# Performance work log

Hardware: AMD Instinct MI355X
Metric: run time of the kernel (lower is better)

## Reference

```python
import jax, jax.numpy as jnp
import numpy as np

HID = 256
NUM_ENT = 100000
NUM_REL = 50
E = 320000  # edges per direction; edge_index has 2*E columns
BN_EPS = 1e-5


def setup_inputs() -> dict:
    key = jax.random.key(0)
    ks = jax.random.split(key, 10)
    x = jax.random.normal(ks[0], (NUM_ENT, HID), dtype=jnp.float32)
    edge_index = jax.random.randint(ks[1], (2, 2 * E), 0, NUM_ENT)
    edge_type = jax.random.randint(ks[2], (2 * E,), 0, NUM_REL)
    rel_embed = jax.random.normal(ks[3], (NUM_REL, HID), dtype=jnp.float32)
    # xavier_normal init: std = sqrt(2 / (fan_in + fan_out))
    w_std = (2.0 / (HID + HID)) ** 0.5
    w_loop = jax.random.normal(ks[4], (HID, HID), dtype=jnp.float32) * w_std
    w_in = jax.random.normal(ks[5], (HID, HID), dtype=jnp.float32) * w_std
    w_out = jax.random.normal(ks[6], (HID, HID), dtype=jnp.float32) * w_std
    w_rel = jax.random.normal(ks[7], (HID, HID), dtype=jnp.float32) * w_std
    loop_rel = jax.random.normal(ks[8], (1, HID), dtype=jnp.float32) * ((2.0 / (1 + HID)) ** 0.5)
    bn_weight = jnp.ones((HID,), dtype=jnp.float32)
    bn_bias = jnp.zeros((HID,), dtype=jnp.float32)
    return {
        "x": x, "edge_index": edge_index, "edge_type": edge_type,
        "rel_embed": rel_embed, "w_loop": w_loop, "w_in": w_in,
        "w_out": w_out, "w_rel": w_rel, "loop_rel": loop_rel,
        "bn_weight": bn_weight, "bn_bias": bn_bias,
    }


def _compute_norm(edge_index, num_ent):
    # symmetric D^-1/2 * D^-1/2 norm; degree counted on row (target) index
    row, col = edge_index[0], edge_index[1]
    deg = jax.ops.segment_sum(jnp.ones_like(row, dtype=jnp.float32), row, num_segments=num_ent)
    deg_inv = jnp.where(deg > 0, deg ** -0.5, 0.0)
    return deg_inv[row] * deg_inv[col]


def _propagate(x, idx, etype, rel_all, W, norm, num_ent):
    # gather source nodes (idx[1]), compose with relation emb (mult), transform, scale, scatter-add to targets (idx[0])
    msg = (x[idx[1]] * rel_all[etype]) @ W  # [E, d]
    if norm is not None:
        msg = msg * norm[:, None]
    return jax.ops.segment_sum(msg, idx[0], num_segments=num_ent)


def reference(x, edge_index, edge_type, rel_embed, w_loop, w_in, w_out, w_rel,
              loop_rel, bn_weight, bn_bias):
    num_ent = x.shape[0]
    rel_all = jnp.concatenate([rel_embed, loop_rel], axis=0)  # [R+1, d]
    e = edge_index.shape[1] // 2
    in_index, out_index = edge_index[:, :e], edge_index[:, e:]
    in_type, out_type = edge_type[:e], edge_type[e:]

    in_norm = _compute_norm(in_index, num_ent)
    out_norm = _compute_norm(out_index, num_ent)

    in_res = _propagate(x, in_index, in_type, rel_all, w_in, in_norm, num_ent)
    out_res = _propagate(x, out_index, out_type, rel_all, w_out, out_norm, num_ent)
    # self-loop: identity scatter -> just per-node compose+transform
    loop_res = (x * loop_rel) @ w_loop

    out = (in_res + out_res + loop_res) * (1.0 / 3.0)

    # BatchNorm1d in training mode (batch stats, biased variance)
    mean = out.mean(axis=0)
    var = out.var(axis=0)
    out = (out - mean) * jax.lax.rsqrt(var + BN_EPS) * bn_weight + bn_bias

    rel_out = (rel_all @ w_rel)[:-1]  # drop loop relation
    return out, rel_out
```

## Files before the change

kernel.cpp:

```cpp
#include <hip/hip_runtime.h>

#define HID     256
#define N_ENT   100000
#define TOT_E   640000
#define HALF_E  320000
#define NSEG    (2 * N_ENT)
#define BN_EPSF 1e-5f
#define SCAN_ELEMS 1024
#define NBLK_SCAN  ((NSEG + SCAN_ELEMS - 1) / SCAN_ELEMS)

typedef short bf16x8 __attribute__((ext_vector_type(8)));
typedef short bf16x4 __attribute__((ext_vector_type(4)));
typedef float f32x4  __attribute__((ext_vector_type(4)));

__device__ __forceinline__ short f2b(float f) {
    union { float f; unsigned u; } c; c.f = f;
    unsigned u = c.u;
    u += 0x7FFF + ((u >> 16) & 1);
    return (short)(u >> 16);
}
__device__ __forceinline__ float b2f(short b) {
    union { unsigned u; float f; } c;
    c.u = ((unsigned)(unsigned short)b) << 16;
    return c.f;
}
__device__ __forceinline__ void gload16(const void* g, void* l) {
    __builtin_amdgcn_global_load_lds(
        (const __attribute__((address_space(1))) unsigned*)(g),
        (__attribute__((address_space(3))) unsigned*)(l), 16, 0, 0);
}

__global__ void hist_kernel(const int* __restrict__ ei, int* __restrict__ offs) {
    int j = blockIdx.x * 256 + threadIdx.x;
    if (j >= TOT_E) return;
    int seg = ei[j] + ((j < HALF_E) ? 0 : N_ENT);
    atomicAdd(&offs[seg], 1);
}

__global__ __launch_bounds__(256) void scan1(int* __restrict__ offs, int* __restrict__ bsums,
                                             float* __restrict__ rnorm) {
    __shared__ int tsum[256];
    int b = blockIdx.x, t = threadIdx.x;
    int base = b * SCAN_ELEMS + t * 4;
    int v[4] = {0, 0, 0, 0};
    if (base + 3 < NSEG) {
        int4 lv = *(const int4*)(offs + base);
        v[0] = lv.x; v[1] = lv.y; v[2] = lv.z; v[3] = lv.w;
    } else {
        for (int i = 0; i < 4; ++i) if (base + i < NSEG) v[i] = offs[base + i];
    }
    #pragma unroll
    for (int i = 0; i < 4; ++i)
        if (base + i < NSEG)
            rnorm[base + i] = (v[i] > 0) ? rsqrtf((float)v[i]) : 0.f;
    tsum[t] = v[0] + v[1] + v[2] + v[3];
    __syncthreads();
    for (int d = 1; d < 256; d <<= 1) {
        int val = (t >= d) ? tsum[t - d] : 0;
        __syncthreads();
        tsum[t] += val;
        __syncthreads();
    }
    int run = (t == 0) ? 0 : tsum[t - 1];
    if (t == 255) bsums[b] = tsum[255];
    int w[4];
    for (int i = 0; i < 4; ++i) { w[i] = run; run += v[i]; }
    if (base + 3 < NSEG) *(int4*)(offs + base) = make_int4(w[0], w[1], w[2], w[3]);
    else for (int i = 0; i < 4; ++i) if (base + i < NSEG) offs[base + i] = w[i];
}

__global__ void scan2(int* __restrict__ bsums) {
    __shared__ int tmp[256];
    int t = threadIdx.x;
    int v = (t < NBLK_SCAN) ? bsums[t] : 0;
    tmp[t] = v;
    __syncthreads();
    for (int d = 1; d < 256; d <<= 1) {
        int val = (t >= d) ? tmp[t - d] : 0;
        __syncthreads();
        tmp[t] += val;
        __syncthreads();
    }
    if (t < NBLK_SCAN) bsums[t] = (t == 0) ? 0 : tmp[t - 1];
}

__global__ __launch_bounds__(256) void scan3(int* __restrict__ offs, const int* __restrict__ bsums) {
    int b = blockIdx.x;
    int add = bsums[b];
    int base = b * SCAN_ELEMS + threadIdx.x * 4;
    if (base + 3 < NSEG) {
        int4 v = *(int4*)(offs + base);
        v.x += add; v.y += add; v.z += add; v.w += add;
        *(int4*)(offs + base) = v;
    } else {
        for (int i = 0; i < 4; ++i) if (base + i < NSEG) offs[base + i] += add;
    }
}

__global__ void fill8_kernel(const int* __restrict__ ei, const int* __restrict__ et,
                             int* __restrict__ offs, const float* __restrict__ rnorm,
                             int2* __restrict__ elist8) {
    int j = blockIdx.x * 256 + threadIdx.x;
    if (j >= TOT_E) return;
    int hb  = (j < HALF_E) ? 0 : N_ENT;
    int seg = ei[j] + hb;
    int col = ei[TOT_E + j];
    float norm = rnorm[seg] * rnorm[hb + col];
    int pos = atomicAdd(&offs[seg], 1);
    elist8[pos] = make_int2(col | (et[j] << 17), __float_as_int(norm));
}

__global__ void tobf16_kernel(const float* __restrict__ src, short* __restrict__ dst, int n8) {
    int i = blockIdx.x * 256 + threadIdx.x;
    if (i >= n8) return;
    const float4* p = (const float4*)(src + (size_t)i * 8);
    float4 v0 = p[0], v1 = p[1];
    bf16x8 pk;
    pk[0]=f2b(v0.x); pk[1]=f2b(v0.y); pk[2]=f2b(v0.z); pk[3]=f2b(v0.w);
    pk[4]=f2b(v1.x); pk[5]=f2b(v1.y); pk[6]=f2b(v1.z); pk[7]=f2b(v1.w);
    *(bf16x8*)(dst + (size_t)i * 8) = pk;
}

__global__ __launch_bounds__(256) void gather_h(
        const short* __restrict__ xh, const short* __restrict__ relh,
        const int* __restrict__ offs, const int2* __restrict__ elist8,
        short* __restrict__ accA, short* __restrict__ accB) {
    int s = blockIdx.x * 8 + (threadIdx.x >> 5);
    int lane = threadIdx.x & 31;
    int start = (s == 0) ? 0 : offs[s - 1];
    int end   = offs[s];
    float a0[8], a1[8];
    #pragma unroll
    for (int k = 0; k < 8; ++k) { a0[k] = 0.f; a1[k] = 0.f; }
    int e = start;
    for (; e + 2 <= end; e += 2) {
        int2 p0 = elist8[e];
        int2 p1 = elist8[e + 1];
        int   c0 = p0.x & 0x1FFFF, t0 = p0.x >> 17;
        float n0 = __int_as_float(p0.y);
        int   c1 = p1.x & 0x1FFFF, t1 = p1.x >> 17;
        float n1 = __int_as_float(p1.y);
        bf16x8 xv0 = *(const bf16x8*)(xh   + (size_t)c0 * HID + lane * 8);
        bf16x8 rv0 = *(const bf16x8*)(relh + (size_t)t0 * HID + lane * 8);
        bf16x8 xv1 = *(const bf16x8*)(xh   + (size_t)c1 * HID + lane * 8);
        bf16x8 rv1 = *(const bf16x8*)(relh + (size_t)t1 * HID + lane * 8);
        #pragma unroll
        for (int k = 0; k < 8; ++k) {
            a0[k] += b2f(xv0[k]) * b2f(rv0[k]) * n0;
            a1[k] += b2f(xv1[k]) * b2f(rv1[k]) * n1;
        }
    }
    if (e < end) {
        int2 p = elist8[e];
        int   c = p.x & 0x1FFFF, t = p.x >> 17;
        float n = __int_as_float(p.y);
        bf16x8 xv = *(const bf16x8*)(xh   + (size_t)c * HID + lane * 8);
        bf16x8 rv = *(const bf16x8*)(relh + (size_t)t * HID + lane * 8);
        #pragma unroll
        for (int k = 0; k < 8; ++k)
            a0[k] += b2f(xv[k]) * b2f(rv[k]) * n;
    }
    int hb = (s >= N_ENT) ? N_ENT : 0;
    short* dst = ((s >= N_ENT) ? accB : accA) + (size_t)(s - hb) * HID + lane * 8;
    bf16x8 pk;
    #pragma unroll
    for (int k = 0; k < 8; ++k) pk[k] = f2b(a0[k] + a1[k]);
    *(bf16x8*)dst = pk;
}

__global__ void wcat_kernel(const float* __restrict__ w_in, const float* __restrict__ w_out,
                            const float* __restrict__ w_loop, const float* __restrict__ loop_rel,
                            short* __restrict__ WT) {
    int n = blockIdx.x;
    int t = threadIdx.x;
    float v0 = w_in  [(size_t)t * HID + n];
    float v1 = w_out [(size_t)t * HID + n];
    float v2 = w_loop[(size_t)t * HID + n] * loop_rel[t];
    short* row = WT + (size_t)n * 768;
    row[t]       = f2b(v0);
    row[256 + t] = f2b(v1);
    row[512 + t] = f2b(v2);
}

template <bool BF16OUT>
__global__ __launch_bounds__(256) void gemm_mfma_db(
        const short* __restrict__ accA, const short* __restrict__ accB,
        const short* __restrict__ xh, const short* __restrict__ WT,
        float* __restrict__ out, short* __restrict__ outh, float* __restrict__ stats)
{
    __shared__ __align__(16) short As[2][64 * 64];
    __shared__ __align__(16) short Bs[2][256 * 64];
    const int tid = threadIdx.x;
    const int l   = tid & 63;
    const int wid = tid >> 6;
    const int r0  = blockIdx.x * 64;
    const int lr  = l & 15;
    const int lg  = l >> 4;

    f32x4 acc[4][4];
    #pragma unroll
    for (int i = 0; i < 4; ++i)
        #pragma unroll
        for (int j = 0; j < 4; ++j)
            acc[i][j] = (f32x4){0.f, 0.f, 0.f, 0.f};

    auto stage = [&](int buf, int kt) {
        const int src = kt >> 2;
        const short* Ap = (src == 0) ? accA : ((src == 1) ? accB : xh);
        const int ksl = (kt & 3) * 64;
        const int ksg = kt * 64;
        #pragma unroll
        for (int h = 0; h < 2; ++h) {
            int c  = wid * 2 + h;
            int r  = c * 8 + (l >> 3);
            int sg = (l & 7) ^ (r & 7);
            int gr = r0 + r;
            if (gr >= N_ENT) gr = N_ENT - 1;
            gload16(Ap + (size_t)gr * HID + ksl + sg * 8, &As[buf][c * 512]);
        }
        #pragma unroll
        for (int i = 0; i < 8; ++i) {
            int c  = wid * 8 + i;
            int n  = c * 8 + (l >> 3);
            int sg = (l & 7) ^ (n & 7);
            gload16(WT + (size_t)n * 768 + ksg + sg * 8, &Bs[buf][c * 512]);
        }
    };

    stage(0, 0);
    __syncthreads();
    int cur = 0;
    for (int kt = 0; kt < 12; ++kt) {
        if (kt < 11) stage(cur ^ 1, kt + 1);
        #pragma unroll
        for (int kc = 0; kc < 2; ++kc) {
            const int gsel = kc * 4 + lg;
            bf16x8 af[4], bfr[4];
            #pragma unroll
            for (int i = 0; i < 4; ++i) {
                int r = 16 * i + lr;
                af[i] = *(const bf16x8*)&As[cur][r * 64 + (gsel ^ (r & 7)) * 8];
            }
            #pragma unroll
            for (int j = 0; j < 4; ++j) {
                int n = wid * 64 + 16 * j + lr;
                bfr[j] = *(const bf16x8*)&Bs[cur][n * 64 + (gsel ^ (n & 7)) * 8];
            }
            #pragma unroll
            for (int i = 0; i < 4; ++i)
                #pragma unroll
                for (int j = 0; j < 4; ++j)
                    acc[i][j] = __builtin_amdgcn_mfma_f32_16x16x32_bf16(
                                    af[i], bfr[j], acc[i][j], 0, 0, 0);
        }
        __syncthreads();
        cur ^= 1;
    }

    const float third = 1.f / 3.f;
    float s[4]  = {0.f, 0.f, 0.f, 0.f};
    float sq[4] = {0.f, 0.f, 0.f, 0.f};
    #pragma unroll
    for (int i = 0; i < 4; ++i) {
        #pragma unroll
        for (int v = 0; v < 4; ++v) {
            int grow = r0 + 16 * i + lg * 4 + v;
            if (grow < N_ENT) {
                #pragma unroll
                for (int j = 0; j < 4; ++j) {
                    float val = acc[i][j][v] * third;
                    int col = wid * 64 + 16 * j + lr;
                    if (BF16OUT) outh[(size_t)grow * HID + col] = f2b(val);
                    else         out [(size_t)grow * HID + col] = val;
                    s[j] += val; sq[j] += val * val;
                }
            }
        }
    }
    #pragma unroll
    for (int j = 0; j < 4; ++j) {
        s[j]  += __shfl_xor(s[j], 16);  s[j]  += __shfl_xor(s[j], 32);
        sq[j] += __shfl_xor(sq[j], 16); sq[j] += __shfl_xor(sq[j], 32);
    }
    if (lg == 0) {
        #pragma unroll
        for (int j = 0; j < 4; ++j) {
            int c = wid * 64 + 16 * j + lr;
            atomicAdd(&stats[c], s[j]);
            atomicAdd(&stats[HID + c], sq[j]);
        }
    }
}

__global__ void bn_apply_h(const short* __restrict__ outh, float* __restrict__ out,
                           const float* __restrict__ stats,
                           const float* __restrict__ bnw, const float* __restrict__ bnb) {
    const float invN = 1.f / (float)N_ENT;
    const int total8 = N_ENT * (HID / 8);
    for (int i = blockIdx.x * 256 + threadIdx.x; i < total8; i += gridDim.x * 256) {
        int c = (i & 31) * 8;
        bf16x8 v = *(const bf16x8*)(outh + (size_t)i * 8);
        float r[8];
        #pragma unroll
        for (int k = 0; k < 8; ++k) {
            float mean = stats[c + k] * invN;
            float var  = stats[HID + c + k] * invN - mean * mean;
            float sc   = rsqrtf(var + BN_EPSF) * bnw[c + k];
            float sh   = bnb[c + k] - mean * sc;
            r[k] = b2f(v[k]) * sc + sh;
        }
        float4* dst = (float4*)(out + (size_t)i * 8);
        dst[0] = make_float4(r[0], r[1], r[2], r[3]);
        dst[1] = make_float4(r[4], r[5], r[6], r[7]);
    }
}

__global__ void bn_apply(float* __restrict__ out, const float* __restrict__ stats,
                         const float* __restrict__ bnw, const float* __restrict__ bnb) {
    const float invN = 1.f / (float)N_ENT;
    const int total4 = N_ENT * (HID / 4);
    for (int i = blockIdx.x * 256 + threadIdx.x; i < total4; i += gridDim.x * 256) {
        int c = (i & 63) * 4;
        float4 v = *(float4*)(out + (size_t)i * 4);
        #pragma unroll
        for (int k = 0; k < 4; ++k) {
            float mean = stats[c + k] * invN;
            float var  = stats[HID + c + k] * invN - mean * mean;
            float sc   = rsqrtf(var + BN_EPSF) * bnw[c + k];
            float sh   = bnb[c + k] - mean * sc;
            float* comp = (k == 0) ? &v.x : (k == 1) ? &v.y : (k == 2) ? &v.z : &v.w;
            *comp = (*comp) * sc + sh;
        }
        *(float4*)(out + (size_t)i * 4) = v;
    }
}

__global__ void relout_kernel(const float* __restrict__ rel_embed,
                              const float* __restrict__ w_rel,
                              float* __restrict__ rel_out) {
    __shared__ float row[HID];
    int r = blockIdx.x;
    int c = threadIdx.x;
    row[c] = rel_embed[(size_t)r * HID + c];
    __syncthreads();
    float s = 0.f;
    for (int k = 0; k < HID; ++k) s += row[k] * w_rel[(size_t)k * HID + c];
    rel_out[(size_t)r * HID + c] = s;
}

extern "C" void kernel_launch(void* const* d_in, const int* in_sizes, int n_in,
                              void* d_out, int out_size, void* d_ws, size_t ws_size,
                              hipStream_t stream) {
    const float* x        = (const float*)d_in[0];
    const int*   ei       = (const int*)d_in[1];
    const int*   et       = (const int*)d_in[2];
    const float* rel      = (const float*)d_in[3];
    const float* w_loop   = (const float*)d_in[4];
    const float* w_in     = (const float*)d_in[5];
    const float* w_out    = (const float*)d_in[6];
    const float* w_rel    = (const float*)d_in[7];
    const float* loop_rel = (const float*)d_in[8];
    const float* bnw      = (const float*)d_in[9];
    const float* bnb      = (const float*)d_in[10];

    float* out     = (float*)d_out;
    float* rel_out = out + (size_t)N_ENT * HID;

    const size_t XH_B   = (size_t)N_ENT * HID * 2;
    const size_t ACC_B  = (size_t)N_ENT * HID * 2;
    const size_t OFFS_B = (size_t)NSEG * 4;
    const size_t EL8_B  = (size_t)TOT_E * 8;
    const size_t RN_B   = (size_t)NSEG * 4;
    const size_t RELH_B = (size_t)50 * HID * 2;
    const size_t base_need = XH_B + 2 * ACC_B + OFFS_B + EL8_B + RN_B
                           + 256 * 4 + 512 * 4 + RELH_B;
    const size_t OUTH_B = (size_t)N_ENT * HID * 2;
    const bool   have_outh = (ws_size >= base_need + OUTH_B);

    char* w = (char*)d_ws;
    short* xh     = (short*)w;              w += XH_B;
    short* accA_h = (short*)w;              w += ACC_B;
    short* accB_h = (short*)w;              w += ACC_B;
    int*   offs   = (int*)w;                w += OFFS_B;
    int2*  elist8 = (int2*)w;               short* WT = (short*)w;   w += EL8_B;
    float* rnorm  = (float*)w;              w += RN_B;
    int*   bsums  = (int*)w;                w += 256 * 4;
    float* stats  = (float*)w;              w += 512 * 4;
    short* relh   = (short*)w;              w += RELH_B;
    short* outh   = (short*)w;

    hipMemsetAsync(offs, 0, OFFS_B, stream);
    hipMemsetAsync(stats, 0, 512 * 4, stream);

    tobf16_kernel<<<(N_ENT * HID / 8 + 255) / 256, 256, 0, stream>>>(x, xh, N_ENT * HID / 8);
    tobf16_kernel<<<(50 * HID / 8 + 255) / 256, 256, 0, stream>>>(rel, relh, 50 * HID / 8);
    hist_kernel<<<TOT_E / 256, 256, 0, stream>>>(ei, offs);
    scan1<<<NBLK_SCAN, 256, 0, stream>>>(offs, bsums, rnorm);
    scan2<<<1, 256, 0, stream>>>(bsums);
    scan3<<<NBLK_SCAN, 256, 0, stream>>>(offs, bsums);
    fill8_kernel<<<TOT_E / 256, 256, 0, stream>>>(ei, et, offs, rnorm, elist8);
    gather_h<<<NSEG / 8, 256, 0, stream>>>(xh, relh, offs, elist8, accA_h, accB_h);
    wcat_kernel<<<256, 256, 0, stream>>>(w_in, w_out, w_loop, loop_rel, WT);
    if (have_outh) {
        gemm_mfma_db<true><<<(N_ENT + 63) / 64, 256, 0, stream>>>(
            accA_h, accB_h, xh, WT, out, outh, stats);
        bn_apply_h<<<2048, 256, 0, stream>>>(outh, out, stats, bnw, bnb);
    } else {
        gemm_mfma_db<false><<<(N_ENT + 63) / 64, 256, 0, stream>>>(
            accA_h, accB_h, xh, WT, out, outh, stats);
        bn_apply<<<2048, 256, 0, stream>>>(out, stats, bnw, bnb);
    }
    relout_kernel<<<50, 256, 0, stream>>>(rel, w_rel, rel_out);
}
```

Measured before the change: 319.3 us.

## Shrink GEMM K-tile, unroll gather by four, merge scan and conversion kernels

Several changes land together. The GEMM K-step drops from 64 to 32, which halves shared memory per block to allow higher occupancy, at the cost of twice as many barriered iterations. The gather loop now handles four edges per iteration to raise memory-level parallelism. The conversion kernels and the scan2/scan3 pair are each fused into one kernel to cut launches, with every scan3 block redoing the small block-sum scan. The BN apply grid is halved and the relout inner loop is unrolled.

```diff
diff --git a/kernel.cpp b/kernel.cpp
--- a/kernel.cpp
+++ b/kernel.cpp
@@ -10,7 +10,6 @@
 #define NBLK_SCAN  ((NSEG + SCAN_ELEMS - 1) / SCAN_ELEMS)
 
 typedef short bf16x8 __attribute__((ext_vector_type(8)));
-typedef short bf16x4 __attribute__((ext_vector_type(4)));
 typedef float f32x4  __attribute__((ext_vector_type(4)));
 
 __device__ __forceinline__ short f2b(float f) {
@@ -69,11 +68,10 @@
     else for (int i = 0; i < 4; ++i) if (base + i < NSEG) offs[base + i] = w[i];
 }
 
-__global__ void scan2(int* __restrict__ bsums) {
+__global__ __launch_bounds__(256) void scan3f(int* __restrict__ offs, const int* __restrict__ bsums) {
     __shared__ int tmp[256];
-    int t = threadIdx.x;
-    int v = (t < NBLK_SCAN) ? bsums[t] : 0;
-    tmp[t] = v;
+    int b = blockIdx.x, t = threadIdx.x;
+    tmp[t] = (t < NBLK_SCAN) ? bsums[t] : 0;
     __syncthreads();
     for (int d = 1; d < 256; d <<= 1) {
         int val = (t >= d) ? tmp[t - d] : 0;
@@ -81,13 +79,8 @@
         tmp[t] += val;
         __syncthreads();
     }
-    if (t < NBLK_SCAN) bsums[t] = (t == 0) ? 0 : tmp[t - 1];
-}
-
-__global__ __launch_bounds__(256) void scan3(int* __restrict__ offs, const int* __restrict__ bsums) {
-    int b = blockIdx.x;
-    int add = bsums[b];
-    int base = b * SCAN_ELEMS + threadIdx.x * 4;
+    int add = (b == 0) ? 0 : tmp[b - 1];
+    int base = b * SCAN_ELEMS + t * 4;
     if (base + 3 < NSEG) {
         int4 v = *(int4*)(offs + base);
         v.x += add; v.y += add; v.z += add; v.w += add;
@@ -110,15 +103,21 @@
     elist8[pos] = make_int2(col | (et[j] << 17), __float_as_int(norm));
 }
 
-__global__ void tobf16_kernel(const float* __restrict__ src, short* __restrict__ dst, int n8) {
+#define NX8 (N_ENT * HID / 8)
+#define NR8 (50 * HID / 8)
+__global__ void tobf16_both(const float* __restrict__ x, short* __restrict__ xh,
+                            const float* __restrict__ rel, short* __restrict__ relh) {
     int i = blockIdx.x * 256 + threadIdx.x;
-    if (i >= n8) return;
-    const float4* p = (const float4*)(src + (size_t)i * 8);
+    const float* src; short* dst; int idx;
+    if (i < NX8) { src = x; dst = xh; idx = i; }
+    else if (i < NX8 + NR8) { src = rel; dst = relh; idx = i - NX8; }
+    else return;
+    const float4* p = (const float4*)(src + (size_t)idx * 8);
     float4 v0 = p[0], v1 = p[1];
     bf16x8 pk;
     pk[0]=f2b(v0.x); pk[1]=f2b(v0.y); pk[2]=f2b(v0.z); pk[3]=f2b(v0.w);
     pk[4]=f2b(v1.x); pk[5]=f2b(v1.y); pk[6]=f2b(v1.z); pk[7]=f2b(v1.w);
-    *(bf16x8*)(dst + (size_t)i * 8) = pk;
+    *(bf16x8*)(dst + (size_t)idx * 8) = pk;
 }
 
 __global__ __launch_bounds__(256) void gather_h(
@@ -129,30 +128,35 @@
     int lane = threadIdx.x & 31;
     int start = (s == 0) ? 0 : offs[s - 1];
     int end   = offs[s];
-    float a0[8], a1[8];
-    #pragma unroll
-    for (int k = 0; k < 8; ++k) { a0[k] = 0.f; a1[k] = 0.f; }
+    float a0[8], a1[8], a2[8], a3[8];
+    #pragma unroll
+    for (int k = 0; k < 8; ++k) { a0[k]=0.f; a1[k]=0.f; a2[k]=0.f; a3[k]=0.f; }
     int e = start;
-    for (; e + 2 <= end; e += 2) {
-        int2 p0 = elist8[e];
-        int2 p1 = elist8[e + 1];
-        int   c0 = p0.x & 0x1FFFF, t0 = p0.x >> 17;
-        float n0 = __int_as_float(p0.y);
-        int   c1 = p1.x & 0x1FFFF, t1 = p1.x >> 17;
-        float n1 = __int_as_float(p1.y);
-        bf16x8 xv0 = *(const bf16x8*)(xh   + (size_t)c0 * HID + lane * 8);
+    for (; e + 4 <= end; e += 4) {
+        int2 p0 = elist8[e], p1 = elist8[e+1], p2 = elist8[e+2], p3 = elist8[e+3];
+        int c0 = p0.x & 0x1FFFF, t0 = p0.x >> 17; float n0 = __int_as_float(p0.y);
+        int c1 = p1.x & 0x1FFFF, t1 = p1.x >> 17; float n1 = __int_as_float(p1.y);
+        int c2 = p2.x & 0x1FFFF, t2 = p2.x >> 17; float n2 = __int_as_float(p2.y);
+        int c3 = p3.x & 0x1FFFF, t3 = p3.x >> 17; float n3 = __int_as_float(p3.y);
+        bf16x8 xv0 = *(const bf16x8*)(xh + (size_t)c0 * HID + lane * 8);
+        bf16x8 xv1 = *(const bf16x8*)(xh + (size_t)c1 * HID + lane * 8);
+        bf16x8 xv2 = *(const bf16x8*)(xh + (size_t)c2 * HID + lane * 8);
+        bf16x8 xv3 = *(const bf16x8*)(xh + (size_t)c3 * HID + lane * 8);
         bf16x8 rv0 = *(const bf16x8*)(relh + (size_t)t0 * HID + lane * 8);
-        bf16x8 xv1 = *(const bf16x8*)(xh   + (size_t)c1 * HID + lane * 8);
         bf16x8 rv1 = *(const bf16x8*)(relh + (size_t)t1 * HID + lane * 8);
+        bf16x8 rv2 = *(const bf16x8*)(relh + (size_t)t2 * HID + lane * 8);
+        bf16x8 rv3 = *(const bf16x8*)(relh + (size_t)t3 * HID + lane * 8);
         #pragma unroll
         for (int k = 0; k < 8; ++k) {
             a0[k] += b2f(xv0[k]) * b2f(rv0[k]) * n0;
             a1[k] += b2f(xv1[k]) * b2f(rv1[k]) * n1;
-        }
-    }
-    if (e < end) {
+            a2[k] += b2f(xv2[k]) * b2f(rv2[k]) * n2;
+            a3[k] += b2f(xv3[k]) * b2f(rv3[k]) * n3;
+        }
+    }
+    for (; e < end; ++e) {
         int2 p = elist8[e];
-        int   c = p.x & 0x1FFFF, t = p.x >> 17;
+        int c = p.x & 0x1FFFF, t = p.x >> 17;
         float n = __int_as_float(p.y);
         bf16x8 xv = *(const bf16x8*)(xh   + (size_t)c * HID + lane * 8);
         bf16x8 rv = *(const bf16x8*)(relh + (size_t)t * HID + lane * 8);
@@ -164,7 +168,7 @@
     short* dst = ((s >= N_ENT) ? accB : accA) + (size_t)(s - hb) * HID + lane * 8;
     bf16x8 pk;
     #pragma unroll
-    for (int k = 0; k < 8; ++k) pk[k] = f2b(a0[k] + a1[k]);
+    for (int k = 0; k < 8; ++k) pk[k] = f2b((a0[k] + a1[k]) + (a2[k] + a3[k]));
     *(bf16x8*)dst = pk;
 }
 
@@ -183,13 +187,13 @@
 }
 
 template <bool BF16OUT>
-__global__ __launch_bounds__(256) void gemm_mfma_db(
+__global__ __launch_bounds__(256) void gemm_mfma_db32(
         const short* __restrict__ accA, const short* __restrict__ accB,
         const short* __restrict__ xh, const short* __restrict__ WT,
         float* __restrict__ out, short* __restrict__ outh, float* __restrict__ stats)
 {
-    __shared__ __align__(16) short As[2][64 * 64];
-    __shared__ __align__(16) short Bs[2][256 * 64];
+    __shared__ __align__(16) short As[2][64 * 32];
+    __shared__ __align__(16) short Bs[2][256 * 32];
     const int tid = threadIdx.x;
     const int l   = tid & 63;
     const int wid = tid >> 6;
@@ -205,54 +209,47 @@
             acc[i][j] = (f32x4){0.f, 0.f, 0.f, 0.f};
 
     auto stage = [&](int buf, int kt) {
-        const int src = kt >> 2;
+        const int src = kt >> 3;
         const short* Ap = (src == 0) ? accA : ((src == 1) ? accB : xh);
-        const int ksl = (kt & 3) * 64;
-        const int ksg = kt * 64;
-        #pragma unroll
-        for (int h = 0; h < 2; ++h) {
-            int c  = wid * 2 + h;
-            int r  = c * 8 + (l >> 3);
-            int sg = (l & 7) ^ (r & 7);
+        const int ksl = (kt & 7) * 32;
+        const int ksg = kt * 32;
+        {
+            int r  = wid * 16 + (l >> 2);
+            int sg = (l & 3) ^ (r & 3);
             int gr = r0 + r;
             if (gr >= N_ENT) gr = N_ENT - 1;
-            gload16(Ap + (size_t)gr * HID + ksl + sg * 8, &As[buf][c * 512]);
-        }
-        #pragma unroll
-        for (int i = 0; i < 8; ++i) {
-            int c  = wid * 8 + i;
-            int n  = c * 8 + (l >> 3);
-            int sg = (l & 7) ^ (n & 7);
-            gload16(WT + (size_t)n * 768 + ksg + sg * 8, &Bs[buf][c * 512]);
+            gload16(Ap + (size_t)gr * HID + ksl + sg * 8, &As[buf][wid * 512]);
+        }
+        #pragma unroll
+        for (int i = 0; i < 4; ++i) {
+            int n  = wid * 64 + i * 16 + (l >> 2);
+            int sg = (l & 3) ^ (n & 3);
+            gload16(WT + (size_t)n * 768 + ksg + sg * 8, &Bs[buf][wid * 2048 + i * 512]);
         }
     };
 
     stage(0, 0);
     __syncthreads();
     int cur = 0;
-    for (int kt = 0; kt < 12; ++kt) {
-        if (kt < 11) stage(cur ^ 1, kt + 1);
-        #pragma unroll
-        for (int kc = 0; kc < 2; ++kc) {
-            const int gsel = kc * 4 + lg;
-            bf16x8 af[4], bfr[4];
+    for (int kt = 0; kt < 24; ++kt) {
+        if (kt < 23) stage(cur ^ 1, kt + 1);
+        bf16x8 af[4], bfr[4];
+        #pragma unroll
+        for (int i = 0; i < 4; ++i) {
+            int r = 16 * i + lr;
+            af[i] = *(const bf16x8*)&As[cur][r * 32 + ((lg ^ (r & 3)) << 3)];
+        }
+        #pragma unroll
+        for (int j = 0; j < 4; ++j) {
+            int n = wid * 64 + 16 * j + lr;
+            bfr[j] = *(const bf16x8*)&Bs[cur][n * 32 + ((lg ^ (n & 3)) << 3)];
+        }
+        #pragma unroll
+        for (int i = 0; i < 4; ++i)
             #pragma unroll
-            for (int i = 0; i < 4; ++i) {
-                int r = 16 * i + lr;
-                af[i] = *(const bf16x8*)&As[cur][r * 64 + (gsel ^ (r & 7)) * 8];
-            }
-            #pragma unroll
-            for (int j = 0; j < 4; ++j) {
-                int n = wid * 64 + 16 * j + lr;
-                bfr[j] = *(const bf16x8*)&Bs[cur][n * 64 + (gsel ^ (n & 7)) * 8];
-            }
-            #pragma unroll
-            for (int i = 0; i < 4; ++i)
-                #pragma unroll
-                for (int j = 0; j < 4; ++j)
-                    acc[i][j] = __builtin_amdgcn_mfma_f32_16x16x32_bf16(
-                                    af[i], bfr[j], acc[i][j], 0, 0, 0);
-        }
+            for (int j = 0; j < 4; ++j)
+                acc[i][j] = __builtin_amdgcn_mfma_f32_16x16x32_bf16(
+                                af[i], bfr[j], acc[i][j], 0, 0, 0);
         __syncthreads();
         cur ^= 1;
     }
@@ -344,6 +341,7 @@
     row[c] = rel_embed[(size_t)r * HID + c];
     __syncthreads();
     float s = 0.f;
+    #pragma unroll 8
     for (int k = 0; k < HID; ++k) s += row[k] * w_rel[(size_t)k * HID + c];
     rel_out[(size_t)r * HID + c] = s;
 }
@@ -392,23 +390,21 @@
     hipMemsetAsync(offs, 0, OFFS_B, stream);
     hipMemsetAsync(stats, 0, 512 * 4, stream);
 
-    tobf16_kernel<<<(N_ENT * HID / 8 + 255) / 256, 256, 0, stream>>>(x, xh, N_ENT * HID / 8);
-    tobf16_kernel<<<(50 * HID / 8 + 255) / 256, 256, 0, stream>>>(rel, relh, 50 * HID / 8);
+    tobf16_both<<<(NX8 + NR8 + 255) / 256, 256, 0, stream>>>(x, xh, rel, relh);
     hist_kernel<<<TOT_E / 256, 256, 0, stream>>>(ei, offs);
     scan1<<<NBLK_SCAN, 256, 0, stream>>>(offs, bsums, rnorm);
-    scan2<<<1, 256, 0, stream>>>(bsums);
-    scan3<<<NBLK_SCAN, 256, 0, stream>>>(offs, bsums);
+    scan3f<<<NBLK_SCAN, 256, 0, stream>>>(offs, bsums);
     fill8_kernel<<<TOT_E / 256, 256, 0, stream>>>(ei, et, offs, rnorm, elist8);
     gather_h<<<NSEG / 8, 256, 0, stream>>>(xh, relh, offs, elist8, accA_h, accB_h);
     wcat_kernel<<<256, 256, 0, stream>>>(w_in, w_out, w_loop, loop_rel, WT);
     if (have_outh) {
-        gemm_mfma_db<true><<<(N_ENT + 63) / 64, 256, 0, stream>>>(
+        gemm_mfma_db32<true><<<(N_ENT + 63) / 64, 256, 0, stream>>>(
             accA_h, accB_h, xh, WT, out, outh, stats);
-        bn_apply_h<<<2048, 256, 0, stream>>>(outh, out, stats, bnw, bnb);
+        bn_apply_h<<<1024, 256, 0, stream>>>(outh, out, stats, bnw, bnb);
     } else {
-        gemm_mfma_db<false><<<(N_ENT + 63) / 64, 256, 0, stream>>>(
+        gemm_mfma_db32<false><<<(N_ENT + 63) / 64, 256, 0, stream>>>(
             accA_h, accB_h, xh, WT, out, outh, stats);
-        bn_apply<<<2048, 256, 0, stream>>>(out, stats, bnw, bnb);
+        bn_apply<<<1024, 256, 0, stream>>>(out, stats, bnw, bnb);
     }
     relout_kernel<<<50, 256, 0, stream>>>(rel, w_rel, rel_out);
 }
```

Result: slower. 354.9 us (+11.2%).
